# Kernel tuning notes

Hardware: AMD Instinct MI355X
Metric: run time of the kernel (lower is better)

## Reference

```python
import jax, jax.numpy as jnp
import numpy as np

H = 1024        # bridge_hidden_dim
NH = 16         # num_attention_heads
HD = H // NH    # head_dim = 64
B, S = 4, 1024
PHYS_W = 0.2
CONS_W = 0.15


def setup_inputs() -> dict:
    key = jax.random.key(0)
    ks = jax.random.split(key, 16)
    sc = 0.02
    return {
        "cnn_features": jax.random.normal(ks[0], (B, S, H), jnp.float32),
        "llm_features": jax.random.normal(ks[1], (B, S, H), jnp.float32),
        "Wq": jax.random.normal(ks[2], (H, H), jnp.float32) * sc,
        "bq": jnp.zeros((H,), jnp.float32),
        "Wk": jax.random.normal(ks[3], (H, H), jnp.float32) * sc,
        "bk": jnp.zeros((H,), jnp.float32),
        "Wv": jax.random.normal(ks[4], (H, H), jnp.float32) * sc,
        "bv": jnp.zeros((H,), jnp.float32),
        "Wo": jax.random.normal(ks[5], (H, H), jnp.float32) * sc,
        "bo": jnp.zeros((H,), jnp.float32),
        "ln_g": jnp.ones((H,), jnp.float32),
        "ln_b": jnp.zeros((H,), jnp.float32),
        "e_energy": jax.random.normal(ks[6], (H,), jnp.float32),
        "e_mass": jax.random.normal(ks[7], (H,), jnp.float32),
        "e_momentum": jax.random.normal(ks[8], (H,), jnp.float32),
    }


def _layernorm(x, g, b, eps=1e-5):
    mu = jnp.mean(x, axis=-1, keepdims=True)
    var = jnp.var(x, axis=-1, keepdims=True)
    return (x - mu) * jax.lax.rsqrt(var + eps) * g + b


def _split_heads(x):
    b, s, _ = x.shape
    return x.reshape(b, s, NH, HD).transpose(0, 2, 1, 3)  # [b, h, s, d]


def _physics_attention(q_in, k_in, v_in, Wq, bq, Wk, bk, Wv, bv, Wo, bo, ln_g, ln_b):
    # q_in: [b, sq, H]; k_in == v_in: [b, sk, H] with sq == sk (required by bias math)
    Q = _split_heads(q_in @ Wq.T + bq)  # [b,h,s,d]
    K = _split_heads(k_in @ Wk.T + bk)
    V = _split_heads(v_in @ Wv.T + bv)
    scores = jnp.einsum('bhqd,bhkd->bhqk', Q, K) / jnp.sqrt(jnp.float32(HD))
    # physics constraints (broadcast [b,h,s,1] over key axis)
    energy_bias = jnp.sum(Q * K, axis=-1, keepdims=True) * PHYS_W
    mass_bias = jnp.mean(Q + K, axis=-1, keepdims=True) * CONS_W
    scores = scores + energy_bias + mass_bias
    attn = jax.nn.softmax(scores, axis=-1)  # dropout is identity in eval
    att = jnp.einsum('bhqk,bhkd->bhqd', attn, V)
    b, h, s, d = att.shape
    att = att.transpose(0, 2, 1, 3).reshape(b, s, h * d)
    out = att @ Wo.T + bo
    return _layernorm(q_in + out, ln_g, ln_b)


def reference(cnn_features, llm_features, Wq, bq, Wk, bk, Wv, bv, Wo, bo,
              ln_g, ln_b, e_energy, e_mass, e_momentum):
    b = cnn_features.shape[0]
    phys = jnp.stack([e_energy, e_mass, e_momentum], axis=0)  # [3, H]
    phys = jnp.broadcast_to(phys[None], (b, 3, H))
    aug_cnn = jnp.concatenate([cnn_features, phys], axis=1)  # [b, S+3, H]
    aug_llm = jnp.concatenate([llm_features, phys], axis=1)
    cnn_att = _physics_attention(aug_cnn, aug_llm, aug_llm,
                                 Wq, bq, Wk, bk, Wv, bv, Wo, bo, ln_g, ln_b)
    llm_att = _physics_attention(aug_llm, aug_cnn, aug_cnn,
                                 Wq, bq, Wk, bk, Wv, bv, Wo, bo, ln_g, ln_b)
    cnn_out = cnn_att[:, :cnn_features.shape[1], :]
    llm_out = llm_att[:, :llm_features.shape[1], :]
    return (cnn_out, llm_out)
```

## Files before the change

### kernel.cpp

```cpp
#include <hip/hip_runtime.h>
#include <stdint.h>

#define SA 1027
#define SPAD 1088

typedef __attribute__((ext_vector_type(8))) short short8;
typedef __attribute__((ext_vector_type(4))) float f32x4;
typedef __attribute__((ext_vector_type(2))) unsigned int u32x2;

typedef const __attribute__((address_space(1))) uint8_t* gas1;
typedef __attribute__((address_space(3))) uint8_t* las3;

__device__ __forceinline__ void gload16(const void* g, void* l){
  __builtin_amdgcn_global_load_lds((gas1)g, (las3)l, 16, 0, 0);
}

__device__ __forceinline__ uint16_t f2bf(float f){
  uint32_t x = __builtin_bit_cast(uint32_t, f);
  x = (x + 0x7fffu + ((x >> 16) & 1u)) >> 16;
  return (uint16_t)x;
}
__device__ __forceinline__ float bf2f(uint16_t u){
  uint32_t x = ((uint32_t)u) << 16;
  return __builtin_bit_cast(float, x);
}

__device__ __forceinline__ f32x4 mfma16(short8 a, short8 b, f32x4 c){
  return __builtin_amdgcn_mfma_f32_16x16x32_bf16(a, b, c, 0, 0, 0);
}

#define QSCALE 0.18033688011112042f

__global__ __launch_bounds__(256) void prep_wb(
    const float* __restrict__ Wq, const float* __restrict__ Wk,
    const float* __restrict__ Wv, const float* __restrict__ Wo,
    const float* __restrict__ bq, const float* __restrict__ bk,
    const float* __restrict__ bv, const float* __restrict__ bo,
    uint16_t* __restrict__ W, float* __restrict__ bias){
  const int gid = blockIdx.x*256 + threadIdx.x;
  if (gid < 1048576){
    const int w = gid >> 18;
    const int off = (gid & 262143) << 2;
    const float* src = (w==0) ? Wq : (w==1) ? Wk : (w==2) ? Wv : Wo;
    const float4 v = *(const float4*)(src + off);
    ushort4 u;
    u.x = f2bf(v.x); u.y = f2bf(v.y); u.z = f2bf(v.z); u.w = f2bf(v.w);
    *(ushort4*)(W + ((size_t)w << 20) + off) = u;
  } else if (gid < 1048576 + 1024){
    const int i = (gid - 1048576) << 2;
    const int w = i >> 10;
    const int off = i & 1023;
    const float* src = (w==0) ? bq : (w==1) ? bk : (w==2) ? bv : bo;
    *(float4*)(bias + i) = *(const float4*)(src + off);
  }
}

__global__ __launch_bounds__(256) void prep_X(
    const float* __restrict__ cnn, const float* __restrict__ llm,
    uint16_t* __restrict__ X){
  const int row = blockIdx.x;
  const int c4 = threadIdx.x << 2;
  const int cb = row >> 10, s = row & 1023;
  const int c = cb >> 2, b = cb & 3;
  const float4 v = *(const float4*)((c ? llm : cnn) + ((size_t)(b*1024 + s))*1024 + c4);
  ushort4 u;
  u.x = f2bf(v.x); u.y = f2bf(v.y); u.z = f2bf(v.z); u.w = f2bf(v.w);
  *(ushort4*)(X + (size_t)row*1024 + c4) = u;
}

__global__ __launch_bounds__(256) void phys_qkv(
    const float* __restrict__ ee, const float* __restrict__ em,
    const float* __restrict__ ep, const uint16_t* __restrict__ W,
    const float* __restrict__ bias, uint16_t* __restrict__ Yqk,
    uint16_t* __restrict__ Vt){
  __shared__ float xs[1024];
  const int t = blockIdx.x >> 3;
  const int col = 1024 + (blockIdx.x & 7)*256 + threadIdx.x;
  const float* e = (t==0) ? ee : (t==1) ? em : ep;
  for (int k = threadIdx.x; k < 1024; k += 256) xs[k] = bf2f(f2bf(e[k]));
  __syncthreads();
  const uint16_t* wr = W + (size_t)col*1024;
  float acc = 0.f;
  for (int k = 0; k < 1024; k += 8){
    const short8 w8 = *(const short8*)(wr + k);
    #pragma unroll
    for (int u = 0; u < 8; ++u) acc += bf2f((uint16_t)w8[u]) * xs[k+u];
  }
  const uint16_t o = f2bf(acc + bias[col]);
  if (col < 2048){
    #pragma unroll
    for (int cb = 0; cb < 8; ++cb)
      Yqk[((size_t)cb*SA + 1024 + t)*2048 + col] = o;
  } else {
    const int hd = col - 2048;
    #pragma unroll
    for (int cb = 0; cb < 8; ++cb)
      Vt[((size_t)(cb*1024 + hd))*SPAD + 1024 + t] = o;
  }
}

__global__ __launch_bounds__(512) void gemm256x128(
    const uint16_t* __restrict__ A, const uint16_t* __restrict__ B,
    const float* __restrict__ bias, uint16_t* __restrict__ C,
    uint16_t* __restrict__ Vt, int K, int lda, int ldb, int ldc,
    int nbn, int mode, float qscale){
  extern __shared__ uint8_t lds[];
  const int tid = threadIdx.x;
  const int lane = tid & 63, wid = tid >> 6;
  const int l15 = lane & 15, l4 = lane >> 4;
  const int wm = wid >> 2, wn = wid & 3;
  const int nwg = gridDim.x;
  const int q8 = nwg >> 3, r8 = nwg & 7;
  const int xcd = blockIdx.x & 7, loc = blockIdx.x >> 3;
  const int wg = (xcd < r8 ? xcd*(q8+1) : r8*(q8+1) + (xcd-r8)*q8) + loc;
  const int bm = wg / nbn, bn = wg % nbn;

  const uint16_t* Ag = A + (size_t)bm*256*lda;
  const uint16_t* Bg = B + (size_t)bn*128*ldb;

  const int srow8 = lane >> 3;
  const int gch = (lane & 7) ^ srow8;
  const int c0 = wid*2, c1 = c0 + 1;
  const size_t ga0 = (size_t)(c0*8 + srow8)*lda + gch*8;
  const size_t ga1 = (size_t)(c1*8 + srow8)*lda + gch*8;
  const size_t gb0 = (size_t)(c0*8 + srow8)*ldb + gch*8;
  const size_t gb1 = (size_t)(c1*8 + srow8)*ldb + gch*8;

#define STG_A(buf, H, kt) do { \
    gload16(Ag + (size_t)(H)*128*lda + (size_t)(kt)*64 + ga0, lds + (buf)*49152 + (H)*16384 + c0*1024); \
    gload16(Ag + (size_t)(H)*128*lda + (size_t)(kt)*64 + ga1, lds + (buf)*49152 + (H)*16384 + c1*1024); \
  } while(0)
#define STG_B(buf, kt) do { \
    gload16(Bg + (size_t)(kt)*64 + gb0, lds + (buf)*49152 + 32768 + c0*1024); \
    gload16(Bg + (size_t)(kt)*64 + gb1, lds + (buf)*49152 + 32768 + c1*1024); \
  } while(0)

  int koff[2];
  koff[0] = (l4*16) ^ ((l15 & 7) << 4);
  koff[1] = (64 + l4*16) ^ ((l15 & 7) << 4);
  const int abase = wm*16384 + l15*128;
  const int bbase = 32768 + (wn*32 + l15)*128;

  f32x4 acc[8][2];
  #pragma unroll
  for (int i = 0; i < 8; ++i){ acc[i][0] = (f32x4){0,0,0,0}; acc[i][1] = (f32x4){0,0,0,0}; }

  const int NT = K >> 6;
  STG_A(0,0,0); STG_A(0,1,0); STG_B(0,0); STG_B(1,1);
  asm volatile("s_waitcnt vmcnt(2)" ::: "memory");
  __builtin_amdgcn_s_barrier();

  for (int s = 0; s < NT; ++s){
    const int b = s & 1, nb = b ^ 1;
    const uint8_t* L = lds + b*49152;
    const int sn1 = (s+1 < NT) ? s+1 : s;
    const int sn2 = (s+2 < NT) ? s+2 : s;
    short8 af[4][2], bfr[2][2];

    #pragma unroll
    for (int i = 0; i < 4; ++i){
      af[i][0] = *(const short8*)(L + abase + i*2048 + koff[0]);
      af[i][1] = *(const short8*)(L + abase + i*2048 + koff[1]);
    }
    #pragma unroll
    for (int j = 0; j < 2; ++j){
      bfr[j][0] = *(const short8*)(L + bbase + j*2048 + koff[0]);
      bfr[j][1] = *(const short8*)(L + bbase + j*2048 + koff[1]);
    }
    STG_A(nb, 0, sn1);
    __builtin_amdgcn_s_barrier();
    asm volatile("s_waitcnt lgkmcnt(0)" ::: "memory");
    __builtin_amdgcn_sched_barrier(0);
    __builtin_amdgcn_s_setprio(1);
    #pragma unroll
    for (int i = 0; i < 4; ++i)
      #pragma unroll
      for (int j = 0; j < 2; ++j)
        acc[i][j] = mfma16(af[i][1], bfr[j][1], mfma16(af[i][0], bfr[j][0], acc[i][j]));
    __builtin_amdgcn_s_setprio(0);
    __builtin_amdgcn_s_barrier();

    #pragma unroll
    for (int i = 0; i < 4; ++i){
      af[i][0] = *(const short8*)(L + abase + 8192 + i*2048 + koff[0]);
      af[i][1] = *(const short8*)(L + abase + 8192 + i*2048 + koff[1]);
    }
    STG_A(nb, 1, sn1);
    STG_B(b, sn2);
    __builtin_amdgcn_s_barrier();
    asm volatile("s_waitcnt lgkmcnt(0)" ::: "memory");
    __builtin_amdgcn_sched_barrier(0);
    __builtin_amdgcn_s_setprio(1);
    #pragma unroll
    for (int i = 0; i < 4; ++i)
      #pragma unroll
      for (int j = 0; j < 2; ++j)
        acc[i+4][j] = mfma16(af[i][1], bfr[j][1], mfma16(af[i][0], bfr[j][0], acc[i+4][j]));
    __builtin_amdgcn_s_setprio(0);
    asm volatile("s_waitcnt vmcnt(2)" ::: "memory");
    __builtin_amdgcn_s_barrier();
  }

  #pragma unroll
  for (int j = 0; j < 2; ++j){
    const int n = bn*128 + wn*32 + j*16 + l15;
    const float bb = bias[n];
    if (mode == 0){
      #pragma unroll
      for (int i = 0; i < 8; ++i){
        const size_t m0 = (size_t)bm*256 + wm*128 + i*16 + l4*4;
        #pragma unroll
        for (int r = 0; r < 4; ++r)
          C[(m0 + r)*ldc + n] = f2bf(acc[i][j][r] + bb);
      }
    } else if (bn < 16){
      const float sc = (n < 1024) ? qscale : 1.0f;
      #pragma unroll
      for (int i = 0; i < 8; ++i){
        const int m0 = bm*256 + wm*128 + i*16 + l4*4;
        #pragma unroll
        for (int r = 0; r < 4; ++r){
          const int m = m0 + r;
          const size_t row = (size_t)(m >> 10)*SA + (m & 1023);
          C[row*2048 + n] = f2bf((acc[i][j][r] + bb) * sc);
        }
      }
    } else {
      const int hd = n - 2048;
      #pragma unroll
      for (int i = 0; i < 8; ++i){
        const int m0 = bm*256 + wm*128 + i*16 + l4*4;
        const size_t vrow = (size_t)(m0 >> 10)*1024 + hd;
        const uint32_t w0 = (uint32_t)f2bf(acc[i][j][0] + bb) | ((uint32_t)f2bf(acc[i][j][1] + bb) << 16);
        const uint32_t w1 = (uint32_t)f2bf(acc[i][j][2] + bb) | ((uint32_t)f2bf(acc[i][j][3] + bb) << 16);
        *(u32x2*)(Vt + vrow*SPAD + (m0 & 1023)) = (u32x2){w0, w1};
      }
    }
  }
#undef STG_A
#undef STG_B
}

__global__ __launch_bounds__(512, 4) void attn_k(
    const uint16_t* __restrict__ Yqk, const uint16_t* __restrict__ Vt,
    uint16_t* __restrict__ att){
  __shared__ __align__(16) uint8_t smK[16384];
  __shared__ __align__(16) uint8_t smV[16384];
  __shared__ __align__(16) uint8_t smP[16384];
  const int tid = threadIdx.x;
  const int lane = tid & 63, wid = tid >> 6;
  const int l15 = lane & 15, l4 = lane >> 4;
  const int i = blockIdx.x;
  const int inst = (i & 7)*16 + ((i >> 3) & 15);
  const int qb = i >> 7;
  const int h = inst & 15, cb = inst >> 4;
  const size_t yrow0 = (size_t)cb * SA;
  const int q0 = qb*256 + wid*32;
  const size_t vbase = (size_t)inst * 64 * SPAD;
  const uint16_t* Yk = Yqk + yrow0*2048 + 1024 + h*64;

  short8 qf[2][2];
  #pragma unroll
  for (int u = 0; u < 2; ++u){
    const uint16_t* p = Yqk + (yrow0 + q0 + u*16 + l15)*2048 + h*64 + l4*8;
    qf[u][0] = *(const short8*)p;
    qf[u][1] = *(const short8*)(p + 32);
  }

  f32x4 o0[4], o1[4];
  float psum0 = 0.f, psum1 = 0.f;
  #pragma unroll
  for (int d = 0; d < 4; ++d){ o0[d] = (f32x4){0,0,0,0}; o1[d] = (f32x4){0,0,0,0}; }

  int koff[2], pwo[4];
  #pragma unroll
  for (int kk = 0; kk < 2; ++kk)
    koff[kk] = (l15*128 + kk*64 + l4*16) ^ ((l15 & 7) << 4);
  #pragma unroll
  for (int nt = 0; nt < 4; ++nt)
    pwo[nt] = (l15*128 + nt*32 + l4*8) ^ ((l15 & 7) << 4);
  uint8_t* const pb = smP + wid*2048;

  const int srow = lane >> 3, schunk = lane & 7;
  const int strow = wid*8 + srow;
  const int sgch = schunk ^ srow;
  {
    gload16(Yk + (size_t)strow*2048 + sgch*8, smK + wid*1024);
    gload16(Vt + vbase + (size_t)strow*SPAD + sgch*8, smV + wid*1024);
  }
  __syncthreads();

  int cur = 0;
  for (int kt = 0; kt < 17; ++kt){
    if (kt < 16){
      const int s1n = (kt + 1)*64;
      const int nb = (cur ^ 1)*8192;
      gload16(Yk + (size_t)(s1n + strow)*2048 + sgch*8, smK + nb + wid*1024);
      gload16(Vt + vbase + (size_t)strow*SPAD + s1n + sgch*8, smV + nb + wid*1024);
    }
    const uint8_t* bK = smK + cur*8192;
    const uint8_t* bV = smV + cur*8192;

    f32x4 sa[4], sb[4];
    #pragma unroll
    for (int nt = 0; nt < 4; ++nt){
      const short8 k0 = *(const short8*)(bK + nt*2048 + koff[0]);
      const short8 k1 = *(const short8*)(bK + nt*2048 + koff[1]);
      sa[nt] = mfma16(k1, qf[0][1], mfma16(k0, qf[0][0], (f32x4){0,0,0,0}));
      sb[nt] = mfma16(k1, qf[1][1], mfma16(k0, qf[1][0], (f32x4){0,0,0,0}));
    }
    if (kt == 16){
      #pragma unroll
      for (int nt = 0; nt < 4; ++nt)
        #pragma unroll
        for (int r = 0; r < 4; ++r){
          if (nt*16 + l4*4 + r >= 3){ sa[nt][r] = -3e38f; sb[nt][r] = -3e38f; }
        }
    }
    #pragma unroll
    for (int nt = 0; nt < 4; ++nt){
      const float p0 = __builtin_amdgcn_exp2f(sa[nt][0]);
      const float p1 = __builtin_amdgcn_exp2f(sa[nt][1]);
      const float p2 = __builtin_amdgcn_exp2f(sa[nt][2]);
      const float p3 = __builtin_amdgcn_exp2f(sa[nt][3]);
      psum0 += (p0 + p1) + (p2 + p3);
      uint32_t w0, w1;
      asm("v_cvt_pk_bf16_f32 %0, %1, %2" : "=v"(w0) : "v"(p0), "v"(p1));
      asm("v_cvt_pk_bf16_f32 %0, %1, %2" : "=v"(w1) : "v"(p2), "v"(p3));
      *(u32x2*)(pb + pwo[nt]) = (u32x2){w0, w1};
    }
    short8 vf[4][2];
    #pragma unroll
    for (int dt = 0; dt < 4; ++dt){
      vf[dt][0] = *(const short8*)(bV + dt*2048 + koff[0]);
      vf[dt][1] = *(const short8*)(bV + dt*2048 + koff[1]);
    }
    #pragma unroll
    for (int kk = 0; kk < 2; ++kk){
      const short8 pf = *(const short8*)(pb + koff[kk]);
      #pragma unroll
      for (int dt = 0; dt < 4; ++dt)
        o0[dt] = mfma16(pf, vf[dt][kk], o0[dt]);
    }
    #pragma unroll
    for (int nt = 0; nt < 4; ++nt){
      const float p0 = __builtin_amdgcn_exp2f(sb[nt][0]);
      const float p1 = __builtin_amdgcn_exp2f(sb[nt][1]);
      const float p2 = __builtin_amdgcn_exp2f(sb[nt][2]);
      const float p3 = __builtin_amdgcn_exp2f(sb[nt][3]);
      psum1 += (p0 + p1) + (p2 + p3);
      uint32_t w0, w1;
      asm("v_cvt_pk_bf16_f32 %0, %1, %2" : "=v"(w0) : "v"(p0), "v"(p1));
      asm("v_cvt_pk_bf16_f32 %0, %1, %2" : "=v"(w1) : "v"(p2), "v"(p3));
      *(u32x2*)(pb + pwo[nt]) = (u32x2){w0, w1};
    }
    #pragma unroll
    for (int kk = 0; kk < 2; ++kk){
      const short8 pf = *(const short8*)(pb + koff[kk]);
      #pragma unroll
      for (int dt = 0; dt < 4; ++dt)
        o1[dt] = mfma16(pf, vf[dt][kk], o1[dt]);
    }
    __syncthreads();
    cur ^= 1;
  }

  psum0 += __shfl_xor(psum0, 16); psum0 += __shfl_xor(psum0, 32);
  psum1 += __shfl_xor(psum1, 16); psum1 += __shfl_xor(psum1, 32);
  const size_t arow0 = (size_t)cb*1024 + q0;
  #pragma unroll
  for (int r = 0; r < 4; ++r){
    const float inv0 = 1.f / __shfl(psum0, l4*4 + r);
    const float inv1 = 1.f / __shfl(psum1, l4*4 + r);
    #pragma unroll
    for (int dt = 0; dt < 4; ++dt){
      att[(arow0 + l4*4 + r)*1024 + h*64 + dt*16 + l15] = f2bf(o0[dt][r] * inv0);
      att[(arow0 + 16 + l4*4 + r)*1024 + h*64 + dt*16 + l15] = f2bf(o1[dt][r] * inv1);
    }
  }
}

__global__ __launch_bounds__(256) void ln_out(
    const uint16_t* __restrict__ Op, const float* __restrict__ cnn,
    const float* __restrict__ llm, const float* __restrict__ g,
    const float* __restrict__ b, float* __restrict__ out){
  const int row = blockIdx.x;
  const int c = row >> 12, bq = row & 4095;
  const int tid = threadIdx.x;
  const ushort4 u = *(const ushort4*)(Op + (size_t)row*1024 + (tid<<2));
  const float4 rv = *(const float4*)((c ? llm : cnn) + (size_t)bq*1024 + (tid<<2));
  const float x0 = bf2f(u.x) + rv.x;
  const float x1 = bf2f(u.y) + rv.y;
  const float x2 = bf2f(u.z) + rv.z;
  const float x3 = bf2f(u.w) + rv.w;
  float s1 = x0+x1+x2+x3;
  float s2 = x0*x0+x1*x1+x2*x2+x3*x3;
  #pragma unroll
  for (int m=1;m<64;m<<=1){ s1 += __shfl_xor(s1,m); s2 += __shfl_xor(s2,m); }
  __shared__ float r1[4], r2[4];
  const int wid = tid >> 6, lane = tid & 63;
  if (lane == 0){ r1[wid] = s1; r2[wid] = s2; }
  __syncthreads();
  s1 = r1[0]+r1[1]+r1[2]+r1[3];
  s2 = r2[0]+r2[1]+r2[2]+r2[3];
  const float mu = s1 * 0.0009765625f;
  const float var = s2 * 0.0009765625f - mu*mu;
  const float rs = rsqrtf(var + 1e-5f);
  const float4 gv = *(const float4*)(g + (tid<<2));
  const float4 bv = *(const float4*)(b + (tid<<2));
  float4 ov;
  ov.x = (x0 - mu)*rs*gv.x + bv.x;
  ov.y = (x1 - mu)*rs*gv.y + bv.y;
  ov.z = (x2 - mu)*rs*gv.z + bv.z;
  ov.w = (x3 - mu)*rs*gv.w + bv.w;
  *(float4*)(out + ((size_t)c << 22) + (size_t)bq*1024 + (tid<<2)) = ov;
}

extern "C" void kernel_launch(void* const* d_in, const int* in_sizes, int n_in,
                              void* d_out, int out_size, void* d_ws, size_t ws_size,
                              hipStream_t stream){
  const float* cnn = (const float*)d_in[0];
  const float* llm = (const float*)d_in[1];
  const float* Wq  = (const float*)d_in[2];
  const float* bq  = (const float*)d_in[3];
  const float* Wk  = (const float*)d_in[4];
  const float* bk  = (const float*)d_in[5];
  const float* Wv  = (const float*)d_in[6];
  const float* bv  = (const float*)d_in[7];
  const float* Wo  = (const float*)d_in[8];
  const float* bo  = (const float*)d_in[9];
  const float* lng = (const float*)d_in[10];
  const float* lnb = (const float*)d_in[11];
  const float* ee  = (const float*)d_in[12];
  const float* em  = (const float*)d_in[13];
  const float* ep  = (const float*)d_in[14];

  uint8_t* ws = (uint8_t*)d_ws;
  uint16_t* X    = (uint16_t*)(ws + 0);
  uint16_t* W    = (uint16_t*)(ws + 16777216);
  float*    bias = (float*)   (ws + 25165824);
  uint16_t* Yqk  = (uint16_t*)(ws + 25182208);
  uint16_t* Vt   = (uint16_t*)(ws + 59785216);
  uint16_t* att  = X;
  uint16_t* Op   = Yqk;
  float* out = (float*)d_out;

  hipFuncSetAttribute((const void*)gemm256x128,
                      hipFuncAttributeMaxDynamicSharedMemorySize, 98304);

  prep_wb<<<4100, 256, 0, stream>>>(Wq, Wk, Wv, Wo, bq, bk, bv, bo, W, bias);
  prep_X<<<8192, 256, 0, stream>>>(cnn, llm, X);
  phys_qkv<<<24, 256, 0, stream>>>(ee, em, ep, W, bias, Yqk, Vt);
  gemm256x128<<<768, 512, 98304, stream>>>(X, W, bias, Yqk, Vt,
                                           1024, 1024, 1024, 2048, 24, 1, QSCALE);
  attn_k<<<512, 512, 0, stream>>>(Yqk, Vt, att);
  gemm256x128<<<256, 512, 98304, stream>>>(att, W + 3145728, bias + 3072, Op, Vt,
                                           1024, 1024, 1024, 1024, 8, 0, 1.0f);
  ln_out<<<8192, 256, 0, stream>>>(Op, cnn, llm, lng, lnb, out);
}
```

Baseline: 184.2 us.

## Use 256x256 tiles for QKV GEMM, specialize O-proj, add MFMA priority in attention

The QKV projection GEMM now uses a 256x256 output tile instead of 256x128, with 128KB of LDS double buffering and a four-phase schedule that interleaves A/B half-tile loads with MFMA groups. This halves the workgroup count to 384, so each workgroup gets more operand reuse and fewer global loads per flop. The output projection gets its own kernel with constants baked in. The attention kernel drops its occupancy hint from launch_bounds and wraps its MFMA sections in s_setprio. The risks are lower occupancy and a tail effect from 384 large tiles on 256 CUs.

```diff
diff --git a/kernel.cpp b/kernel.cpp
--- a/kernel.cpp
+++ b/kernel.cpp
@@ -99,73 +99,72 @@
   }
 }
 
-__global__ __launch_bounds__(512) void gemm256x128(
+__global__ __launch_bounds__(512) void qkv256(
     const uint16_t* __restrict__ A, const uint16_t* __restrict__ B,
-    const float* __restrict__ bias, uint16_t* __restrict__ C,
-    uint16_t* __restrict__ Vt, int K, int lda, int ldb, int ldc,
-    int nbn, int mode, float qscale){
+    const float* __restrict__ bias, uint16_t* __restrict__ Yqk,
+    uint16_t* __restrict__ Vt){
   extern __shared__ uint8_t lds[];
   const int tid = threadIdx.x;
   const int lane = tid & 63, wid = tid >> 6;
   const int l15 = lane & 15, l4 = lane >> 4;
   const int wm = wid >> 2, wn = wid & 3;
-  const int nwg = gridDim.x;
-  const int q8 = nwg >> 3, r8 = nwg & 7;
-  const int xcd = blockIdx.x & 7, loc = blockIdx.x >> 3;
-  const int wg = (xcd < r8 ? xcd*(q8+1) : r8*(q8+1) + (xcd-r8)*q8) + loc;
-  const int bm = wg / nbn, bn = wg % nbn;
-
-  const uint16_t* Ag = A + (size_t)bm*256*lda;
-  const uint16_t* Bg = B + (size_t)bn*128*ldb;
+  const int wg = (blockIdx.x & 7)*48 + (blockIdx.x >> 3);
+  const int bm = wg / 12, bn = wg % 12;
+
+  const uint16_t* Ag = A + (size_t)bm*256*1024;
+  const uint16_t* Bg = B + (size_t)bn*256*1024;
 
   const int srow8 = lane >> 3;
   const int gch = (lane & 7) ^ srow8;
   const int c0 = wid*2, c1 = c0 + 1;
-  const size_t ga0 = (size_t)(c0*8 + srow8)*lda + gch*8;
-  const size_t ga1 = (size_t)(c1*8 + srow8)*lda + gch*8;
-  const size_t gb0 = (size_t)(c0*8 + srow8)*ldb + gch*8;
-  const size_t gb1 = (size_t)(c1*8 + srow8)*ldb + gch*8;
+  const size_t ga0 = (size_t)(c0*8 + srow8)*1024 + gch*8;
+  const size_t ga1 = (size_t)(c1*8 + srow8)*1024 + gch*8;
 
 #define STG_A(buf, H, kt) do { \
-    gload16(Ag + (size_t)(H)*128*lda + (size_t)(kt)*64 + ga0, lds + (buf)*49152 + (H)*16384 + c0*1024); \
-    gload16(Ag + (size_t)(H)*128*lda + (size_t)(kt)*64 + ga1, lds + (buf)*49152 + (H)*16384 + c1*1024); \
+    gload16(Ag + (size_t)(H)*131072 + (size_t)(kt)*64 + ga0, lds + (buf)*65536 + (H)*16384 + c0*1024); \
+    gload16(Ag + (size_t)(H)*131072 + (size_t)(kt)*64 + ga1, lds + (buf)*65536 + (H)*16384 + c1*1024); \
   } while(0)
-#define STG_B(buf, kt) do { \
-    gload16(Bg + (size_t)(kt)*64 + gb0, lds + (buf)*49152 + 32768 + c0*1024); \
-    gload16(Bg + (size_t)(kt)*64 + gb1, lds + (buf)*49152 + 32768 + c1*1024); \
+#define STG_B(buf, H, kt) do { \
+    gload16(Bg + (size_t)(H)*131072 + (size_t)(kt)*64 + ga0, lds + (buf)*65536 + 32768 + (H)*16384 + c0*1024); \
+    gload16(Bg + (size_t)(H)*131072 + (size_t)(kt)*64 + ga1, lds + (buf)*65536 + 32768 + (H)*16384 + c1*1024); \
   } while(0)
 
   int koff[2];
   koff[0] = (l4*16) ^ ((l15 & 7) << 4);
   koff[1] = (64 + l4*16) ^ ((l15 & 7) << 4);
-  const int abase = wm*16384 + l15*128;
-  const int bbase = 32768 + (wn*32 + l15)*128;
-
-  f32x4 acc[8][2];
-  #pragma unroll
-  for (int i = 0; i < 8; ++i){ acc[i][0] = (f32x4){0,0,0,0}; acc[i][1] = (f32x4){0,0,0,0}; }
-
-  const int NT = K >> 6;
-  STG_A(0,0,0); STG_A(0,1,0); STG_B(0,0); STG_B(1,1);
-  asm volatile("s_waitcnt vmcnt(2)" ::: "memory");
+  const int arow = (wm*128 + l15) * 128;
+  const int brow = (wn*64 + l15) * 128;
+
+  f32x4 acc[8][4];
+  #pragma unroll
+  for (int i = 0; i < 8; ++i)
+    #pragma unroll
+    for (int j = 0; j < 4; ++j) acc[i][j] = (f32x4){0.f,0.f,0.f,0.f};
+
+  const int NT = 16;
+  STG_A(0,0,0); STG_A(0,1,0); STG_B(0,0,0); STG_B(0,1,0);
+  STG_B(1,0,1); STG_B(1,1,1);
+  asm volatile("s_waitcnt vmcnt(4)" ::: "memory");
   __builtin_amdgcn_s_barrier();
 
   for (int s = 0; s < NT; ++s){
-    const int b = s & 1, nb = b ^ 1;
-    const uint8_t* L = lds + b*49152;
+    const int b = s & 1;
+    const uint8_t* La = lds + b*65536;
+    const uint8_t* Lb = La + 32768;
     const int sn1 = (s+1 < NT) ? s+1 : s;
     const int sn2 = (s+2 < NT) ? s+2 : s;
-    short8 af[4][2], bfr[2][2];
+    const int nb = b ^ 1;
+    short8 af[4][2], bf0[2][2], bf1[2][2];
 
     #pragma unroll
     for (int i = 0; i < 4; ++i){
-      af[i][0] = *(const short8*)(L + abase + i*2048 + koff[0]);
-      af[i][1] = *(const short8*)(L + abase + i*2048 + koff[1]);
+      af[i][0] = *(const short8*)(La + arow + i*2048 + koff[0]);
+      af[i][1] = *(const short8*)(La + arow + i*2048 + koff[1]);
     }
     #pragma unroll
     for (int j = 0; j < 2; ++j){
-      bfr[j][0] = *(const short8*)(L + bbase + j*2048 + koff[0]);
-      bfr[j][1] = *(const short8*)(L + bbase + j*2048 + koff[1]);
+      bf0[j][0] = *(const short8*)(Lb + brow + j*2048 + koff[0]);
+      bf0[j][1] = *(const short8*)(Lb + brow + j*2048 + koff[1]);
     }
     STG_A(nb, 0, sn1);
     __builtin_amdgcn_s_barrier();
@@ -176,17 +175,16 @@
     for (int i = 0; i < 4; ++i)
       #pragma unroll
       for (int j = 0; j < 2; ++j)
-        acc[i][j] = mfma16(af[i][1], bfr[j][1], mfma16(af[i][0], bfr[j][0], acc[i][j]));
-    __builtin_amdgcn_s_setprio(0);
-    __builtin_amdgcn_s_barrier();
-
-    #pragma unroll
-    for (int i = 0; i < 4; ++i){
-      af[i][0] = *(const short8*)(L + abase + 8192 + i*2048 + koff[0]);
-      af[i][1] = *(const short8*)(L + abase + 8192 + i*2048 + koff[1]);
+        acc[i][j] = mfma16(af[i][1], bf0[j][1], mfma16(af[i][0], bf0[j][0], acc[i][j]));
+    __builtin_amdgcn_s_setprio(0);
+    __builtin_amdgcn_s_barrier();
+
+    #pragma unroll
+    for (int j = 0; j < 2; ++j){
+      bf1[j][0] = *(const short8*)(Lb + brow + (j+2)*2048 + koff[0]);
+      bf1[j][1] = *(const short8*)(Lb + brow + (j+2)*2048 + koff[1]);
     }
     STG_A(nb, 1, sn1);
-    STG_B(b, sn2);
     __builtin_amdgcn_s_barrier();
     asm volatile("s_waitcnt lgkmcnt(0)" ::: "memory");
     __builtin_amdgcn_sched_barrier(0);
@@ -195,34 +193,54 @@
     for (int i = 0; i < 4; ++i)
       #pragma unroll
       for (int j = 0; j < 2; ++j)
-        acc[i+4][j] = mfma16(af[i][1], bfr[j][1], mfma16(af[i][0], bfr[j][0], acc[i+4][j]));
-    __builtin_amdgcn_s_setprio(0);
-    asm volatile("s_waitcnt vmcnt(2)" ::: "memory");
-    __builtin_amdgcn_s_barrier();
-  }
-
-  #pragma unroll
-  for (int j = 0; j < 2; ++j){
-    const int n = bn*128 + wn*32 + j*16 + l15;
+        acc[i][j+2] = mfma16(af[i][1], bf1[j][1], mfma16(af[i][0], bf1[j][0], acc[i][j+2]));
+    __builtin_amdgcn_s_setprio(0);
+    __builtin_amdgcn_s_barrier();
+
+    #pragma unroll
+    for (int i = 0; i < 4; ++i){
+      af[i][0] = *(const short8*)(La + 8192 + arow + i*2048 + koff[0]);
+      af[i][1] = *(const short8*)(La + 8192 + arow + i*2048 + koff[1]);
+    }
+    STG_B(b, 0, sn2);
+    __builtin_amdgcn_s_barrier();
+    asm volatile("s_waitcnt lgkmcnt(0)" ::: "memory");
+    __builtin_amdgcn_sched_barrier(0);
+    __builtin_amdgcn_s_setprio(1);
+    #pragma unroll
+    for (int i = 0; i < 4; ++i)
+      #pragma unroll
+      for (int j = 0; j < 2; ++j)
+        acc[i+4][j+2] = mfma16(af[i][1], bf1[j][1], mfma16(af[i][0], bf1[j][0], acc[i+4][j+2]));
+    __builtin_amdgcn_s_setprio(0);
+    __builtin_amdgcn_s_barrier();
+
+    STG_B(b, 1, sn2);
+    __builtin_amdgcn_s_barrier();
+    __builtin_amdgcn_s_setprio(1);
+    #pragma unroll
+    for (int i = 0; i < 4; ++i)
+      #pragma unroll
+      for (int j = 0; j < 2; ++j)
+        acc[i+4][j] = mfma16(af[i][1], bf0[j][1], mfma16(af[i][0], bf0[j][0], acc[i+4][j]));
+    __builtin_amdgcn_s_setprio(0);
+    asm volatile("s_waitcnt vmcnt(4)" ::: "memory");
+    __builtin_amdgcn_s_barrier();
+  }
+
+  #pragma unroll
+  for (int j = 0; j < 4; ++j){
+    const int n = bn*256 + wn*64 + j*16 + l15;
     const float bb = bias[n];
-    if (mode == 0){
-      #pragma unroll
-      for (int i = 0; i < 8; ++i){
-        const size_t m0 = (size_t)bm*256 + wm*128 + i*16 + l4*4;
-        #pragma unroll
-        for (int r = 0; r < 4; ++r)
-          C[(m0 + r)*ldc + n] = f2bf(acc[i][j][r] + bb);
-      }
-    } else if (bn < 16){
-      const float sc = (n < 1024) ? qscale : 1.0f;
+    if (n < 2048){
+      const float sc = (n < 1024) ? QSCALE : 1.0f;
       #pragma unroll
       for (int i = 0; i < 8; ++i){
         const int m0 = bm*256 + wm*128 + i*16 + l4*4;
         #pragma unroll
         for (int r = 0; r < 4; ++r){
           const int m = m0 + r;
-          const size_t row = (size_t)(m >> 10)*SA + (m & 1023);
-          C[row*2048 + n] = f2bf((acc[i][j][r] + bb) * sc);
+          Yqk[((size_t)(m >> 10)*SA + (m & 1023))*2048 + n] = f2bf((acc[i][j][r] + bb) * sc);
         }
       }
     } else {
@@ -241,7 +259,118 @@
 #undef STG_B
 }
 
-__global__ __launch_bounds__(512, 4) void attn_k(
+__global__ __launch_bounds__(512) void oproj256(
+    const uint16_t* __restrict__ A, const uint16_t* __restrict__ B,
+    const float* __restrict__ bias, uint16_t* __restrict__ C){
+  extern __shared__ uint8_t lds[];
+  const int tid = threadIdx.x;
+  const int lane = tid & 63, wid = tid >> 6;
+  const int l15 = lane & 15, l4 = lane >> 4;
+  const int wm = wid >> 2, wn = wid & 3;
+  const int wg = (blockIdx.x & 7)*32 + (blockIdx.x >> 3);
+  const int bm = wg >> 3, bn = wg & 7;
+
+  const uint16_t* Ag = A + (size_t)bm*256*1024;
+  const uint16_t* Bg = B + (size_t)bn*128*1024;
+
+  const int srow8 = lane >> 3;
+  const int gch = (lane & 7) ^ srow8;
+  const int c0 = wid*2, c1 = c0 + 1;
+  const size_t ga0 = (size_t)(c0*8 + srow8)*1024 + gch*8;
+  const size_t ga1 = (size_t)(c1*8 + srow8)*1024 + gch*8;
+
+#define STG_A(buf, H, kt) do { \
+    gload16(Ag + (size_t)(H)*131072 + (size_t)(kt)*64 + ga0, lds + (buf)*49152 + (H)*16384 + c0*1024); \
+    gload16(Ag + (size_t)(H)*131072 + (size_t)(kt)*64 + ga1, lds + (buf)*49152 + (H)*16384 + c1*1024); \
+  } while(0)
+#define STG_B(buf, kt) do { \
+    gload16(Bg + (size_t)(kt)*64 + ga0, lds + (buf)*49152 + 32768 + c0*1024); \
+    gload16(Bg + (size_t)(kt)*64 + ga1, lds + (buf)*49152 + 32768 + c1*1024); \
+  } while(0)
+
+  int koff[2];
+  koff[0] = (l4*16) ^ ((l15 & 7) << 4);
+  koff[1] = (64 + l4*16) ^ ((l15 & 7) << 4);
+  const int abase = wm*16384 + l15*128;
+  const int bbase = 32768 + (wn*32 + l15)*128;
+
+  f32x4 acc[8][2];
+  #pragma unroll
+  for (int i = 0; i < 8; ++i){ acc[i][0] = (f32x4){0,0,0,0}; acc[i][1] = (f32x4){0,0,0,0}; }
+
+  const int NT = 16;
+  STG_A(0,0,0); STG_A(0,1,0); STG_B(0,0); STG_B(1,1);
+  asm volatile("s_waitcnt vmcnt(2)" ::: "memory");
+  __builtin_amdgcn_s_barrier();
+
+  for (int s = 0; s < NT; ++s){
+    const int b = s & 1, nb = b ^ 1;
+    const uint8_t* L = lds + b*49152;
+    const int sn1 = (s+1 < NT) ? s+1 : s;
+    const int sn2 = (s+2 < NT) ? s+2 : s;
+    short8 af[4][2], bfr[2][2];
+
+    #pragma unroll
+    for (int i = 0; i < 4; ++i){
+      af[i][0] = *(const short8*)(L + abase + i*2048 + koff[0]);
+      af[i][1] = *(const short8*)(L + abase + i*2048 + koff[1]);
+    }
+    #pragma unroll
+    for (int j = 0; j < 2; ++j){
+      bfr[j][0] = *(const short8*)(L + bbase + j*2048 + koff[0]);
+      bfr[j][1] = *(const short8*)(L + bbase + j*2048 + koff[1]);
+    }
+    STG_A(nb, 0, sn1);
+    __builtin_amdgcn_s_barrier();
+    asm volatile("s_waitcnt lgkmcnt(0)" ::: "memory");
+    __builtin_amdgcn_sched_barrier(0);
+    __builtin_amdgcn_s_setprio(1);
+    #pragma unroll
+    for (int i = 0; i < 4; ++i)
+      #pragma unroll
+      for (int j = 0; j < 2; ++j)
+        acc[i][j] = mfma16(af[i][1], bfr[j][1], mfma16(af[i][0], bfr[j][0], acc[i][j]));
+    __builtin_amdgcn_s_setprio(0);
+    __builtin_amdgcn_s_barrier();
+
+    #pragma unroll
+    for (int i = 0; i < 4; ++i){
+      af[i][0] = *(const short8*)(L + abase + 8192 + i*2048 + koff[0]);
+      af[i][1] = *(const short8*)(L + abase + 8192 + i*2048 + koff[1]);
+    }
+    STG_A(nb, 1, sn1);
+    STG_B(b, sn2);
+    __builtin_amdgcn_s_barrier();
+    asm volatile("s_waitcnt lgkmcnt(0)" ::: "memory");
+    __builtin_amdgcn_sched_barrier(0);
+    __builtin_amdgcn_s_setprio(1);
+    #pragma unroll
+    for (int i = 0; i < 4; ++i)
+      #pragma unroll
+      for (int j = 0; j < 2; ++j)
+        acc[i+4][j] = mfma16(af[i][1], bfr[j][1], mfma16(af[i][0], bfr[j][0], acc[i+4][j]));
+    __builtin_amdgcn_s_setprio(0);
+    asm volatile("s_waitcnt vmcnt(2)" ::: "memory");
+    __builtin_amdgcn_s_barrier();
+  }
+
+  #pragma unroll
+  for (int j = 0; j < 2; ++j){
+    const int n = bn*128 + wn*32 + j*16 + l15;
+    const float bb = bias[n];
+    #pragma unroll
+    for (int i = 0; i < 8; ++i){
+      const size_t m0 = (size_t)bm*256 + wm*128 + i*16 + l4*4;
+      #pragma unroll
+      for (int r = 0; r < 4; ++r)
+        C[(m0 + r)*1024 + n] = f2bf(acc[i][j][r] + bb);
+    }
+  }
+#undef STG_A
+#undef STG_B
+}
+
+__global__ __launch_bounds__(512) void attn_k(
     const uint16_t* __restrict__ Yqk, const uint16_t* __restrict__ Vt,
     uint16_t* __restrict__ att){
   __shared__ __align__(16) uint8_t smK[16384];
@@ -302,6 +431,7 @@
     const uint8_t* bV = smV + cur*8192;
 
     f32x4 sa[4], sb[4];
+    __builtin_amdgcn_s_setprio(1);
     #pragma unroll
     for (int nt = 0; nt < 4; ++nt){
       const short8 k0 = *(const short8*)(bK + nt*2048 + koff[0]);
@@ -309,6 +439,7 @@
       sa[nt] = mfma16(k1, qf[0][1], mfma16(k0, qf[0][0], (f32x4){0,0,0,0}));
       sb[nt] = mfma16(k1, qf[1][1], mfma16(k0, qf[1][0], (f32x4){0,0,0,0}));
     }
+    __builtin_amdgcn_s_setprio(0);
     if (kt == 16){
       #pragma unroll
       for (int nt = 0; nt < 4; ++nt)
@@ -335,6 +466,7 @@
       vf[dt][0] = *(const short8*)(bV + dt*2048 + koff[0]);
       vf[dt][1] = *(const short8*)(bV + dt*2048 + koff[1]);
     }
+    __builtin_amdgcn_s_setprio(1);
     #pragma unroll
     for (int kk = 0; kk < 2; ++kk){
       const short8 pf = *(const short8*)(pb + koff[kk]);
@@ -342,6 +474,7 @@
       for (int dt = 0; dt < 4; ++dt)
         o0[dt] = mfma16(pf, vf[dt][kk], o0[dt]);
     }
+    __builtin_amdgcn_s_setprio(0);
     #pragma unroll
     for (int nt = 0; nt < 4; ++nt){
       const float p0 = __builtin_amdgcn_exp2f(sb[nt][0]);
@@ -354,6 +487,7 @@
       asm("v_cvt_pk_bf16_f32 %0, %1, %2" : "=v"(w1) : "v"(p2), "v"(p3));
       *(u32x2*)(pb + pwo[nt]) = (u32x2){w0, w1};
     }
+    __builtin_amdgcn_s_setprio(1);
     #pragma unroll
     for (int kk = 0; kk < 2; ++kk){
       const short8 pf = *(const short8*)(pb + koff[kk]);
@@ -361,6 +495,7 @@
       for (int dt = 0; dt < 4; ++dt)
         o1[dt] = mfma16(pf, vf[dt][kk], o1[dt]);
     }
+    __builtin_amdgcn_s_setprio(0);
     __syncthreads();
     cur ^= 1;
   }
@@ -445,16 +580,16 @@
   uint16_t* Op   = Yqk;
   float* out = (float*)d_out;
 
-  hipFuncSetAttribute((const void*)gemm256x128,
+  hipFuncSetAttribute((const void*)qkv256,
+                      hipFuncAttributeMaxDynamicSharedMemorySize, 131072);
+  hipFuncSetAttribute((const void*)oproj256,
                       hipFuncAttributeMaxDynamicSharedMemorySize, 98304);
 
   prep_wb<<<4100, 256, 0, stream>>>(Wq, Wk, Wv, Wo, bq, bk, bv, bo, W, bias);
   prep_X<<<8192, 256, 0, stream>>>(cnn, llm, X);
   phys_qkv<<<24, 256, 0, stream>>>(ee, em, ep, W, bias, Yqk, Vt);
-  gemm256x128<<<768, 512, 98304, stream>>>(X, W, bias, Yqk, Vt,
-                                           1024, 1024, 1024, 2048, 24, 1, QSCALE);
+  qkv256<<<384, 512, 131072, stream>>>(X, W, bias, Yqk, Vt);
   attn_k<<<512, 512, 0, stream>>>(Yqk, Vt, att);
-  gemm256x128<<<256, 512, 98304, stream>>>(att, W + 3145728, bias + 3072, Op, Vt,
-                                           1024, 1024, 1024, 1024, 8, 0, 1.0f);
+  oproj256<<<256, 512, 98304, stream>>>(att, W + 3145728, bias + 3072, Op);
   ln_out<<<8192, 256, 0, stream>>>(Op, cnn, llm, lng, lnb, out);
 }
```

Result: slower. 199.2 us (+8.2%).
